# Performance work log

Hardware: AMD Instinct MI355X
Metric: run time of the kernel (lower is better)

The kernel has to match this reference:

```python
import jax, jax.numpy as jnp
import numpy as np

NUM_HEADS = 16


def setup_inputs() -> dict:
    key = jax.random.key(0)
    kx, kp, kq, kw, kb = jax.random.split(key, 5)
    B, N, C = 2, 2048, 1024
    x = jax.random.normal(kx, (B, N, C), dtype=jnp.float32)
    padding_mask = jax.random.randint(kp, (B, N), 0, 2).astype(jnp.bool_)
    W_qkv = jax.random.normal(kq, (C, 3 * C), dtype=jnp.float32) * (C ** -0.5)
    W_proj = jax.random.normal(kw, (C, C), dtype=jnp.float32) * (C ** -0.5)
    b_proj = jax.random.normal(kb, (C,), dtype=jnp.float32) * 0.02
    return {"x": x, "padding_mask": padding_mask, "causal_start": 128,
            "W_qkv": W_qkv, "W_proj": W_proj, "b_proj": b_proj}


def reference(x, padding_mask, causal_start, W_qkv, W_proj, b_proj):
    B, N, C = x.shape
    H = NUM_HEADS
    d = C // H
    scale = d ** -0.5
    # qkv projection: (B,N,3C) -> (3,B,H,N,d)
    qkv = (x @ W_qkv).reshape(B, N, 3, H, d).transpose(2, 0, 3, 1, 4)
    q, k, v = qkv[0], qkv[1], qkv[2]
    attn = jnp.einsum("bhqd,bhkd->bhqk", q * scale, k)  # (B,H,N,N)
    # padding mask: mask out padded KEY positions
    attn = jnp.where(padding_mask[:, None, None, :], -jnp.inf, attn)
    # offset causal mask: lower-triangular, but first `causal_start` columns always visible
    allowed = jnp.tril(jnp.ones((N, N), dtype=jnp.bool_))
    allowed = allowed | (jnp.arange(N)[None, :] < causal_start)
    attn = jnp.where(~allowed[None, None, :, :], -jnp.inf, attn)
    attn = jax.nn.softmax(attn.astype(jnp.float32), axis=-1).astype(x.dtype)
    out = jnp.einsum("bhqk,bhkd->bhqd", attn, v)  # (B,H,N,d)
    out = out.transpose(0, 2, 1, 3).reshape(B, N, C)
    return out @ W_proj + b_proj
```

## Files before the change

kernel.cpp:

```cpp
#include <hip/hip_runtime.h>
#include <stdint.h>

typedef unsigned short ushort_t;
typedef __attribute__((ext_vector_type(4))) unsigned short ushort4_t;
typedef __attribute__((ext_vector_type(8))) short short8;
typedef __attribute__((ext_vector_type(4))) float float4_t;

#define AS1 __attribute__((address_space(1)))
#define AS3 __attribute__((address_space(3)))

__device__ inline ushort_t f2bf(float f) {
    unsigned x = __builtin_bit_cast(unsigned, f);
    unsigned r = x + 0x7fffu + ((x >> 16) & 1u);
    return (ushort_t)(r >> 16);
}
__device__ inline ushort_t f2bf_trunc(float f) {
    return (ushort_t)(__builtin_bit_cast(unsigned, f) >> 16);
}

__global__ __launch_bounds__(256) void prep_fused(
    const float* __restrict__ wqkv, const float* __restrict__ x,
    const int* __restrict__ pad, const float* __restrict__ wproj,
    ushort_t* __restrict__ wqkvT, ushort_t* __restrict__ xbf,
    int* __restrict__ tbl, ushort_t* __restrict__ wprojT) {
    __shared__ __align__(16) ushort_t tile[64][65];
    __shared__ int wsum[4];
    int bid = blockIdx.x, t = threadIdx.x;
    if (bid < 768) {
        int bx = bid % 48, by = bid / 48;
        int c0 = bx * 64, r0 = by * 64;
        for (int i = 0; i < 16; i++) {
            int idx = t + i * 256;
            int lr = idx >> 6, lc = idx & 63;
            tile[lr][lc] = f2bf(wqkv[(size_t)(r0 + lr) * 3072 + c0 + lc]);
        }
        __syncthreads();
        for (int i = 0; i < 16; i++) {
            int idx = t + i * 256;
            int lr = idx >> 6, lc = idx & 63;
            wqkvT[(size_t)(c0 + lr) * 1024 + r0 + lc] = tile[lc][lr];
        }
    } else if (bid < 2816) {
        size_t i = ((size_t)(bid - 768) * 256 + t) * 8;
        float4_t a = *(const float4_t*)(x + i);
        float4_t b = *(const float4_t*)(x + i + 4);
        ushort_t u[8];
        u[0] = f2bf(a.x); u[1] = f2bf(a.y); u[2] = f2bf(a.z); u[3] = f2bf(a.w);
        u[4] = f2bf(b.x); u[5] = f2bf(b.y); u[6] = f2bf(b.z); u[7] = f2bf(b.w);
        *(ushort4_t*)(xbf + i) = *(ushort4_t*)&u[0];
        *(ushort4_t*)(xbf + i + 4) = *(ushort4_t*)&u[4];
    } else if (bid < 2818) {
        int b = bid - 2816;
        int* cvtab = tbl;
        int* pref = tbl + 4096;
        int* idxmap = tbl + 8192;
        int* vcp = tbl + 12288;
        int lane = t & 63, w4 = t >> 6;
        int base0 = t * 8;
        int v[8], s8 = 0;
        for (int j = 0; j < 8; j++) {
            v[j] = (pad[b * 2048 + base0 + j] == 0) ? 1 : 0;
            s8 += v[j];
        }
        int incl = s8;
        for (int off = 1; off < 64; off <<= 1) {
            int y = __shfl_up(incl, off, 64);
            if (lane >= off) incl += y;
        }
        int excl = incl - s8;
        if (lane == 63) wsum[w4] = incl;
        __syncthreads();
        int wbase = 0;
        for (int ww = 0; ww < 4; ww++) if (ww < w4) wbase += wsum[ww];
        int vcall = wsum[0] + wsum[1] + wsum[2] + wsum[3];
        int run = wbase + excl;
        for (int j = 0; j < 8; j++) {
            int pos = base0 + j;
            pref[b * 2048 + pos] = run;
            cvtab[b * 2048 + pos] = v[j] ? run : -1;
            if (v[j]) idxmap[b * 2048 + run] = pos;
            run += v[j];
        }
        if (t == 0) vcp[b] = vcall;
        for (int s = vcall + t; s < 2048; s += 256) idxmap[b * 2048 + s] = 2048;
    } else {
        int tid2 = bid - 2818;
        int c0 = (tid2 & 15) * 64, r0 = (tid2 >> 4) * 64;
        for (int i = 0; i < 16; i++) {
            int idx = t + i * 256;
            int lr = idx >> 6, lc = idx & 63;
            tile[lr][lc] = f2bf(wproj[(size_t)(r0 + lr) * 1024 + c0 + lc]);
        }
        __syncthreads();
        for (int i = 0; i < 16; i++) {
            int idx = t + i * 256;
            int lr = idx >> 6, lc = idx & 63;
            wprojT[(size_t)(c0 + lr) * 1024 + r0 + lc] = tile[lc][lr];
        }
    }
}

__global__ __launch_bounds__(256) void transpose_f32_bf16(const float* __restrict__ in,
                                                          ushort_t* __restrict__ out,
                                                          int R, int C) {
    __shared__ __align__(16) ushort_t tile[64][65];
    int c0 = blockIdx.x * 64, r0 = blockIdx.y * 64;
    int t = threadIdx.x;
    for (int i = 0; i < 16; i++) {
        int idx = t + i * 256;
        int lr = idx >> 6, lc = idx & 63;
        tile[lr][lc] = f2bf(in[(size_t)(r0 + lr) * C + c0 + lc]);
    }
    __syncthreads();
    for (int i = 0; i < 16; i++) {
        int idx = t + i * 256;
        int lr = idx >> 6, lc = idx & 63;
        out[(size_t)(c0 + lr) * R + r0 + lc] = tile[lc][lr];
    }
}

__global__ __launch_bounds__(256) void gemm_qkv(
    const ushort_t* __restrict__ A, const ushort_t* __restrict__ Bt,
    const int* __restrict__ tbl,
    ushort_t* __restrict__ outQ, ushort_t* __restrict__ outK, ushort_t* __restrict__ outV) {
    const int K = 1024;
    __shared__ __align__(16) ushort_t As[128 * 64];
    __shared__ __align__(16) ushort_t Bs[128 * 64];
    const int* idxmap = tbl + 8192;
    const int* vcp = tbl + 12288;
    int t = threadIdx.x;
    int w = t >> 6, lane = t & 63;
    int quad = lane >> 4, l15 = lane & 15;
    int wM = w >> 1, wN = w & 1;
    int lrow = lane >> 3;
    int lcol8 = (lane & 7) * 8;

    int wid = blockIdx.x + 24 * blockIdx.y;
    bool isQ = wid < 256;
    int b = 0, m0, vc = 0, tNr;
    size_t arow[4];
    if (isQ) {
        tNr = (wid & 7) * 128;
        m0 = (wid >> 3) * 128;
        for (int i = 0; i < 4; i++)
            arow[i] = (size_t)(m0 + w * 32 + i * 8 + lrow) * K;
    } else {
        int idx = wid - 256;
        int grp = idx >> 8;
        int r = idx & 255;
        int xkv = r >> 4;
        b = (r >> 3) & 1;
        int st = (r & 7) + grp * 8;
        tNr = 1024 + xkv * 128;
        vc = vcp[b];
        m0 = st * 128;
        if (m0 >= vc) return;
        for (int i = 0; i < 4; i++) {
            int slot = m0 + w * 32 + i * 8 + lrow;
            int orig = idxmap[b * 2048 + slot];
            arow[i] = (size_t)(b * 2048 + orig) * K;
        }
    }

    float4_t acc[4][4];
    for (int i = 0; i < 4; i++)
        for (int j = 0; j < 4; j++) acc[i][j] = (float4_t){0.f, 0.f, 0.f, 0.f};

    const ushort_t* Bbase = Bt + (size_t)(tNr + w * 32) * K;

    for (int k0 = 0; k0 < K; k0 += 64) {
        __syncthreads();
        for (int i = 0; i < 4; i++) {
            const ushort_t* ga = A + arow[i] + k0 + lcol8;
            __builtin_amdgcn_global_load_lds((AS1 void*)ga, (AS3 void*)&As[(w * 32 + i * 8) * 64], 16, 0, 0);
            const ushort_t* gb = Bbase + (size_t)(i * 8 + lrow) * K + k0 + lcol8;
            __builtin_amdgcn_global_load_lds((AS1 void*)gb, (AS3 void*)&Bs[(w * 32 + i * 8) * 64], 16, 0, 0);
        }
        __syncthreads();
        for (int kt = 0; kt < 2; kt++) {
            short8 af[4], bf[4];
            for (int m = 0; m < 4; m++)
                af[m] = *(const short8*)&As[(wM * 64 + m * 16 + l15) * 64 + kt * 32 + quad * 8];
            for (int n = 0; n < 4; n++)
                bf[n] = *(const short8*)&Bs[(wN * 64 + n * 16 + l15) * 64 + kt * 32 + quad * 8];
            for (int m = 0; m < 4; m++)
                for (int n = 0; n < 4; n++)
                    acc[m][n] = __builtin_amdgcn_mfma_f32_16x16x32_bf16(af[m], bf[n], acc[m][n], 0, 0, 0);
        }
    }

    for (int m = 0; m < 4; m++) {
        int lm = wM * 64 + m * 16 + quad * 4;
        for (int n = 0; n < 4; n++) {
            int lnc = wN * 64 + n * 16 + l15;
            if (isQ) {
                int gn = tNr + lnc;
                int h = gn >> 6, dd = gn & 63;
                for (int r = 0; r < 4; r++) {
                    int row = m0 + lm + r;
                    int bb = row >> 11, ns = row & 2047;
                    outQ[(((size_t)(bb * 16 + h) * 2048 + ns) << 6) + dd] = f2bf(acc[m][n][r]);
                }
            } else {
                int gnc = tNr - 1024 + lnc;
                ushort_t* dst = (gnc < 1024) ? outK : outV;
                int hh = (gnc >> 6) & 15, dd = gnc & 63;
                for (int r = 0; r < 4; r++) {
                    int slot = m0 + lm + r;
                    if (slot < vc)
                        dst[(((size_t)(b * 16 + hh) * 2048 + slot) << 6) + dd] = f2bf(acc[m][n][r]);
                }
            }
        }
    }
}

__global__ __launch_bounds__(512, 4) void attn_kernel(
    const ushort_t* __restrict__ q, const ushort_t* __restrict__ k,
    const ushort_t* __restrict__ v, const int* __restrict__ tbl,
    const int* __restrict__ csp, ushort_t* __restrict__ out) {
    __shared__ __align__(16) ushort_t Ks[2][64 * 64];
    __shared__ __align__(16) ushort_t VsT[2][64 * 64];
    __shared__ __align__(16) ushort_t Ps[8][16 * 64];
    __shared__ int Idx[2048];

    const int* pref = tbl + 4096;
    const int* idxmap = tbl + 8192;
    const int* vcp = tbl + 12288;

    int cs = csp[0];
    int t = threadIdx.x, w = t >> 6, lane = t & 63;
    int quad = lane >> 4, l15 = lane & 15;
    int bh = blockIdx.y;
    int b = bh >> 4, h = bh & 15;
    int g = (blockIdx.y < 16) ? blockIdx.x : 15 - blockIdx.x;
    int q0 = g * 128;
    int rowmin = q0 + w * 16;
    const float c1 = 0.18033688f;
    const float c2 = -11.541560f;

    int bound = q0 + 128; if (cs > bound) bound = cs;
    int nvalid = (bound > 2047) ? vcp[b] : pref[b * 2048 + bound];
    int nT = (nvalid + 63) >> 6; if (nT < 1) nT = 1;

    for (int i = 0; i < 4; i++) Idx[t + i * 512] = idxmap[b * 2048 + t + i * 512];

    const ushort_t* qb = q + ((size_t)bh * 2048 + rowmin + l15) * 64;
    short8 qf0 = *(const short8*)(qb + quad * 8);
    short8 qf1 = *(const short8*)(qb + 32 + quad * 8);

    float4_t O[4];
    for (int i = 0; i < 4; i++) O[i] = (float4_t){0.f, 0.f, 0.f, 0.f};
    float ls[4] = {0.f, 0.f, 0.f, 0.f};

    const ushort_t* kbase = k + (size_t)bh * 2048 * 64;
    const ushort_t* vbase = v + (size_t)bh * 2048 * 64;

    int lrow = lane >> 3, lblk = lane & 7;
    int prow = rowmin + quad * 4;
    int sw = l15 & 7;

    short8 vr;
    auto stageK = [&](int it, int buf) {
        int k0 = it * 64;
        const ushort_t* gk = kbase + (size_t)(k0 + w * 8 + lrow) * 64 + ((lblk ^ lrow) * 8);
        __builtin_amdgcn_global_load_lds((AS1 void*)gk, (AS3 void*)&Ks[buf][w * 8 * 64], 16, 0, 0);
    };
    auto loadV = [&](int it) {
        vr = *(const short8*)(vbase + (size_t)(it * 64 + lane) * 64 + w * 8);
        if (it * 64 + lane >= nvalid)
            for (int j = 0; j < 8; j++) vr[j] = 0;
    };

    stageK(0, 0);
    loadV(0);

    for (int it = 0; it < nT; it++) {
        int cur = it & 1, nxt = cur ^ 1;
        for (int j = 0; j < 8; j++) {
            int sl = ((lrow ^ j) * 8) + lblk;
            VsT[cur][(w * 8 + j) * 64 + sl] = (ushort_t)vr[j];
        }
        __syncthreads();
        if (it + 1 < nT) {
            stageK(it + 1, nxt);
            loadV(it + 1);
        }

        int k0 = it * 64;
        int omin = Idx[k0];
        bool act = (omin <= rowmin + 15) || (omin < cs);
        if (act) {
            int omax = Idx[k0 + 63];
            bool needC = (omax > rowmin) && (omax >= cs);

            short8 kf0[4], kf1[4];
            for (int ks = 0; ks < 4; ks++) {
                const ushort_t* krow = &Ks[cur][(ks * 16 + l15) * 64];
                kf0[ks] = *(const short8*)(krow + (quad ^ sw) * 8);
                kf1[ks] = *(const short8*)(krow + ((4 + quad) ^ sw) * 8);
            }

            float4_t s[4];
            for (int ks = 0; ks < 4; ks++) {
                float4_t a = (float4_t){0.f, 0.f, 0.f, 0.f};
                a = __builtin_amdgcn_mfma_f32_16x16x32_bf16(qf0, kf0[ks], a, 0, 0, 0);
                a = __builtin_amdgcn_mfma_f32_16x16x32_bf16(qf1, kf1[ks], a, 0, 0, 0);
                s[ks] = a;
            }
            for (int ks = 0; ks < 4; ks++) {
                int key = Idx[k0 + ks * 16 + l15];
                for (int r = 0; r < 4; r++) {
                    float arg = s[ks][r] * c1 + c2;
                    if (needC && (key > prow + r) && (key >= cs)) arg = -1e38f;
                    float p = __builtin_amdgcn_exp2f(arg);
                    ls[r] += p;
                    int row = quad * 4 + r;
                    Ps[w][row * 64 + (((ks * 2 + (l15 >> 3)) ^ (row & 7)) * 8) + (l15 & 7)] = f2bf_trunc(p);
                }
            }

            short8 vf0[4], vf1[4];
            for (int n = 0; n < 4; n++) {
                const ushort_t* vrow = &VsT[cur][(n * 16 + l15) * 64];
                vf0[n] = *(const short8*)(vrow + (quad ^ sw) * 8);
                vf1[n] = *(const short8*)(vrow + ((4 + quad) ^ sw) * 8);
            }
            const ushort_t* prl = &Ps[w][l15 * 64];
            short8 pf0 = *(const short8*)(prl + (quad ^ sw) * 8);
            short8 pf1 = *(const short8*)(prl + ((4 + quad) ^ sw) * 8);
            for (int n = 0; n < 4; n++) {
                O[n] = __builtin_amdgcn_mfma_f32_16x16x32_bf16(pf0, vf0[n], O[n], 0, 0, 0);
                O[n] = __builtin_amdgcn_mfma_f32_16x16x32_bf16(pf1, vf1[n], O[n], 0, 0, 0);
            }
        }
    }

    for (int r = 0; r < 4; r++) {
        float l = ls[r];
        l += __shfl_xor(l, 1, 64); l += __shfl_xor(l, 2, 64);
        l += __shfl_xor(l, 4, 64); l += __shfl_xor(l, 8, 64);
        float inv = l > 0.f ? 1.f / l : 0.f;
        int row = rowmin + quad * 4 + r;
        size_t ob = ((size_t)b * 2048 + row) * 1024 + h * 64;
        for (int n = 0; n < 4; n++)
            out[ob + n * 16 + l15] = f2bf(O[n][r] * inv);
    }
}

__global__ __launch_bounds__(256) void gemm_out_k(
    const ushort_t* __restrict__ A, const ushort_t* __restrict__ Bt,
    const float* __restrict__ bias, float* __restrict__ outC) {
    const int K = 1024, N = 1024;
    __shared__ __align__(16) ushort_t As[128 * 64];
    __shared__ __align__(16) ushort_t Bs[128 * 64];
    int t = threadIdx.x;
    int w = t >> 6, lane = t & 63;
    int quad = lane >> 4, l15 = lane & 15;
    int wM = w >> 1, wN = w & 1;
    int tM = blockIdx.y * 128, tN = blockIdx.x * 128;

    float4_t acc[4][4];
    for (int i = 0; i < 4; i++)
        for (int j = 0; j < 4; j++) acc[i][j] = (float4_t){0.f, 0.f, 0.f, 0.f};

    int lrow = lane >> 3;
    int lcol8 = (lane & 7) * 8;

    const ushort_t* Abase = A + (size_t)(tM + w * 32) * K;
    const ushort_t* Bbase = Bt + (size_t)(tN + w * 32) * K;

    for (int k0 = 0; k0 < K; k0 += 64) {
        __syncthreads();
        for (int i = 0; i < 4; i++) {
            const ushort_t* ga = Abase + (size_t)(i * 8 + lrow) * K + k0 + lcol8;
            __builtin_amdgcn_global_load_lds((AS1 void*)ga, (AS3 void*)&As[(w * 32 + i * 8) * 64], 16, 0, 0);
            const ushort_t* gb = Bbase + (size_t)(i * 8 + lrow) * K + k0 + lcol8;
            __builtin_amdgcn_global_load_lds((AS1 void*)gb, (AS3 void*)&Bs[(w * 32 + i * 8) * 64], 16, 0, 0);
        }
        __syncthreads();
        for (int kt = 0; kt < 2; kt++) {
            short8 af[4], bf[4];
            for (int m = 0; m < 4; m++)
                af[m] = *(const short8*)&As[(wM * 64 + m * 16 + l15) * 64 + kt * 32 + quad * 8];
            for (int n = 0; n < 4; n++)
                bf[n] = *(const short8*)&Bs[(wN * 64 + n * 16 + l15) * 64 + kt * 32 + quad * 8];
            for (int m = 0; m < 4; m++)
                for (int n = 0; n < 4; n++)
                    acc[m][n] = __builtin_amdgcn_mfma_f32_16x16x32_bf16(af[m], bf[n], acc[m][n], 0, 0, 0);
        }
    }

    for (int m = 0; m < 4; m++) {
        int gm = tM + wM * 64 + m * 16 + quad * 4;
        for (int n = 0; n < 4; n++) {
            int gn = tN + wN * 64 + n * 16 + l15;
            float bv = bias[gn];
            for (int r = 0; r < 4; r++)
                outC[(size_t)(gm + r) * N + gn] = acc[m][n][r] + bv;
        }
    }
}

extern "C" void kernel_launch(void* const* d_in, const int* in_sizes, int n_in,
                              void* d_out, int out_size, void* d_ws, size_t ws_size,
                              hipStream_t stream) {
    const float* x = (const float*)d_in[0];
    const int* pad = (const int*)d_in[1];
    const int* cs = (const int*)d_in[2];
    const float* wqkv = (const float*)d_in[3];
    const float* wproj = (const float*)d_in[4];
    const float* bproj = (const float*)d_in[5];
    float* out = (float*)d_out;

    ushort_t* ws = (ushort_t*)d_ws;
    ushort_t* qws = ws;
    ushort_t* kws = ws + (size_t)4194304;
    ushort_t* vws = ws + (size_t)8388608;
    ushort_t* wqkvT = ws + (size_t)12582912;
    ushort_t* aows = ws + (size_t)12582912;
    ushort_t* xbf = (ushort_t*)d_out;
    int* tbl = (int*)((char*)d_out + 8388608);

    bool fused_wp = ws_size >= (size_t)34 * 1024 * 1024;
    ushort_t* wprojT = fused_wp ? ws + (size_t)16777216 : ws;

    prep_fused<<<fused_wp ? 3074 : 2818, 256, 0, stream>>>(wqkv, x, pad, wproj,
                                                           wqkvT, xbf, tbl, wprojT);
    gemm_qkv<<<dim3(24, 32), 256, 0, stream>>>(xbf, wqkvT, tbl, qws, kws, vws);
    attn_kernel<<<dim3(16, 32), 512, 0, stream>>>(qws, kws, vws, tbl, cs, aows);
    if (!fused_wp)
        transpose_f32_bf16<<<dim3(16, 16), 256, 0, stream>>>(wproj, wprojT, 1024, 1024);
    gemm_out_k<<<dim3(8, 32), 256, 0, stream>>>(aows, wprojT, bproj, out);
}
```

Baseline: 175.3 us.

## Split K across two wave groups in projection GEMMs with LDS reduction

Both the QKV and output-projection GEMMs now launch 512-thread blocks. Two groups of four waves each handle one half of the K dimension in separate LDS buffers, then combine their partial accumulators through shared memory before the epilogue. This doubles the waves per tile to improve latency hiding and halves the serial K loop per wave. The cost is twice the LDS per block (64KB), an extra reduction step with two barriers, and possibly lower block-level occupancy.

After: 174.5 us. Within noise of the previous version (-0.5%).

```diff
diff --git a/kernel.cpp b/kernel.cpp
--- a/kernel.cpp
+++ b/kernel.cpp
@@ -119,19 +119,19 @@
     }
 }
 
-__global__ __launch_bounds__(256) void gemm_qkv(
+__global__ __launch_bounds__(512, 4) void gemm_qkv(
     const ushort_t* __restrict__ A, const ushort_t* __restrict__ Bt,
     const int* __restrict__ tbl,
     ushort_t* __restrict__ outQ, ushort_t* __restrict__ outK, ushort_t* __restrict__ outV) {
     const int K = 1024;
-    __shared__ __align__(16) ushort_t As[128 * 64];
-    __shared__ __align__(16) ushort_t Bs[128 * 64];
+    __shared__ __align__(16) ushort_t smem[4][128 * 64];
     const int* idxmap = tbl + 8192;
     const int* vcp = tbl + 12288;
     int t = threadIdx.x;
     int w = t >> 6, lane = t & 63;
+    int wq = w & 3, kh = w >> 2;
     int quad = lane >> 4, l15 = lane & 15;
-    int wM = w >> 1, wN = w & 1;
+    int wM = wq >> 1, wN = wq & 1;
     int lrow = lane >> 3;
     int lcol8 = (lane & 7) * 8;
 
@@ -143,7 +143,7 @@
         tNr = (wid & 7) * 128;
         m0 = (wid >> 3) * 128;
         for (int i = 0; i < 4; i++)
-            arow[i] = (size_t)(m0 + w * 32 + i * 8 + lrow) * K;
+            arow[i] = (size_t)(m0 + wq * 32 + i * 8 + lrow) * K;
     } else {
         int idx = wid - 256;
         int grp = idx >> 8;
@@ -156,7 +156,7 @@
         m0 = st * 128;
         if (m0 >= vc) return;
         for (int i = 0; i < 4; i++) {
-            int slot = m0 + w * 32 + i * 8 + lrow;
+            int slot = m0 + wq * 32 + i * 8 + lrow;
             int orig = idxmap[b * 2048 + slot];
             arow[i] = (size_t)(b * 2048 + orig) * K;
         }
@@ -166,28 +166,45 @@
     for (int i = 0; i < 4; i++)
         for (int j = 0; j < 4; j++) acc[i][j] = (float4_t){0.f, 0.f, 0.f, 0.f};
 
-    const ushort_t* Bbase = Bt + (size_t)(tNr + w * 32) * K;
-
-    for (int k0 = 0; k0 < K; k0 += 64) {
+    const ushort_t* Bbase = Bt + (size_t)(tNr + wq * 32) * K;
+    const int kb = kh * 512;
+
+    for (int k0 = 0; k0 < 512; k0 += 64) {
         __syncthreads();
         for (int i = 0; i < 4; i++) {
-            const ushort_t* ga = A + arow[i] + k0 + lcol8;
-            __builtin_amdgcn_global_load_lds((AS1 void*)ga, (AS3 void*)&As[(w * 32 + i * 8) * 64], 16, 0, 0);
-            const ushort_t* gb = Bbase + (size_t)(i * 8 + lrow) * K + k0 + lcol8;
-            __builtin_amdgcn_global_load_lds((AS1 void*)gb, (AS3 void*)&Bs[(w * 32 + i * 8) * 64], 16, 0, 0);
+            const ushort_t* ga = A + arow[i] + kb + k0 + lcol8;
+            __builtin_amdgcn_global_load_lds((AS1 void*)ga, (AS3 void*)&smem[kh][(wq * 32 + i * 8) * 64], 16, 0, 0);
+            const ushort_t* gb = Bbase + (size_t)(i * 8 + lrow) * K + kb + k0 + lcol8;
+            __builtin_amdgcn_global_load_lds((AS1 void*)gb, (AS3 void*)&smem[2 + kh][(wq * 32 + i * 8) * 64], 16, 0, 0);
         }
         __syncthreads();
         for (int kt = 0; kt < 2; kt++) {
             short8 af[4], bf[4];
             for (int m = 0; m < 4; m++)
-                af[m] = *(const short8*)&As[(wM * 64 + m * 16 + l15) * 64 + kt * 32 + quad * 8];
+                af[m] = *(const short8*)&smem[kh][(wM * 64 + m * 16 + l15) * 64 + kt * 32 + quad * 8];
             for (int n = 0; n < 4; n++)
-                bf[n] = *(const short8*)&Bs[(wN * 64 + n * 16 + l15) * 64 + kt * 32 + quad * 8];
+                bf[n] = *(const short8*)&smem[2 + kh][(wN * 64 + n * 16 + l15) * 64 + kt * 32 + quad * 8];
             for (int m = 0; m < 4; m++)
                 for (int n = 0; n < 4; n++)
                     acc[m][n] = __builtin_amdgcn_mfma_f32_16x16x32_bf16(af[m], bf[n], acc[m][n], 0, 0, 0);
         }
     }
+
+    __syncthreads();
+    float4_t* red = (float4_t*)smem;
+    if (kh == 1) {
+        for (int m = 0; m < 4; m++)
+            for (int n = 0; n < 4; n++)
+                red[(wq * 16 + m * 4 + n) * 64 + lane] = acc[m][n];
+    }
+    __syncthreads();
+    if (kh == 1) return;
+    for (int m = 0; m < 4; m++)
+        for (int n = 0; n < 4; n++) {
+            float4_t o = red[(wq * 16 + m * 4 + n) * 64 + lane];
+            acc[m][n].x += o.x; acc[m][n].y += o.y;
+            acc[m][n].z += o.z; acc[m][n].w += o.w;
+        }
 
     for (int m = 0; m < 4; m++) {
         int lm = wM * 64 + m * 16 + quad * 4;
@@ -348,16 +365,16 @@
     }
 }
 
-__global__ __launch_bounds__(256) void gemm_out_k(
+__global__ __launch_bounds__(512, 4) void gemm_out_k(
     const ushort_t* __restrict__ A, const ushort_t* __restrict__ Bt,
     const float* __restrict__ bias, float* __restrict__ outC) {
     const int K = 1024, N = 1024;
-    __shared__ __align__(16) ushort_t As[128 * 64];
-    __shared__ __align__(16) ushort_t Bs[128 * 64];
+    __shared__ __align__(16) ushort_t smem[4][128 * 64];
     int t = threadIdx.x;
     int w = t >> 6, lane = t & 63;
+    int wq = w & 3, kh = w >> 2;
     int quad = lane >> 4, l15 = lane & 15;
-    int wM = w >> 1, wN = w & 1;
+    int wM = wq >> 1, wN = wq & 1;
     int tM = blockIdx.y * 128, tN = blockIdx.x * 128;
 
     float4_t acc[4][4];
@@ -367,29 +384,46 @@
     int lrow = lane >> 3;
     int lcol8 = (lane & 7) * 8;
 
-    const ushort_t* Abase = A + (size_t)(tM + w * 32) * K;
-    const ushort_t* Bbase = Bt + (size_t)(tN + w * 32) * K;
-
-    for (int k0 = 0; k0 < K; k0 += 64) {
+    const ushort_t* Abase = A + (size_t)(tM + wq * 32) * K;
+    const ushort_t* Bbase = Bt + (size_t)(tN + wq * 32) * K;
+    const int kb = kh * 512;
+
+    for (int k0 = 0; k0 < 512; k0 += 64) {
         __syncthreads();
         for (int i = 0; i < 4; i++) {
-            const ushort_t* ga = Abase + (size_t)(i * 8 + lrow) * K + k0 + lcol8;
-            __builtin_amdgcn_global_load_lds((AS1 void*)ga, (AS3 void*)&As[(w * 32 + i * 8) * 64], 16, 0, 0);
-            const ushort_t* gb = Bbase + (size_t)(i * 8 + lrow) * K + k0 + lcol8;
-            __builtin_amdgcn_global_load_lds((AS1 void*)gb, (AS3 void*)&Bs[(w * 32 + i * 8) * 64], 16, 0, 0);
+            const ushort_t* ga = Abase + (size_t)(i * 8 + lrow) * K + kb + k0 + lcol8;
+            __builtin_amdgcn_global_load_lds((AS1 void*)ga, (AS3 void*)&smem[kh][(wq * 32 + i * 8) * 64], 16, 0, 0);
+            const ushort_t* gb = Bbase + (size_t)(i * 8 + lrow) * K + kb + k0 + lcol8;
+            __builtin_amdgcn_global_load_lds((AS1 void*)gb, (AS3 void*)&smem[2 + kh][(wq * 32 + i * 8) * 64], 16, 0, 0);
         }
         __syncthreads();
         for (int kt = 0; kt < 2; kt++) {
             short8 af[4], bf[4];
             for (int m = 0; m < 4; m++)
-                af[m] = *(const short8*)&As[(wM * 64 + m * 16 + l15) * 64 + kt * 32 + quad * 8];
+                af[m] = *(const short8*)&smem[kh][(wM * 64 + m * 16 + l15) * 64 + kt * 32 + quad * 8];
             for (int n = 0; n < 4; n++)
-                bf[n] = *(const short8*)&Bs[(wN * 64 + n * 16 + l15) * 64 + kt * 32 + quad * 8];
+                bf[n] = *(const short8*)&smem[2 + kh][(wN * 64 + n * 16 + l15) * 64 + kt * 32 + quad * 8];
             for (int m = 0; m < 4; m++)
                 for (int n = 0; n < 4; n++)
                     acc[m][n] = __builtin_amdgcn_mfma_f32_16x16x32_bf16(af[m], bf[n], acc[m][n], 0, 0, 0);
         }
     }
+
+    __syncthreads();
+    float4_t* red = (float4_t*)smem;
+    if (kh == 1) {
+        for (int m = 0; m < 4; m++)
+            for (int n = 0; n < 4; n++)
+                red[(wq * 16 + m * 4 + n) * 64 + lane] = acc[m][n];
+    }
+    __syncthreads();
+    if (kh == 1) return;
+    for (int m = 0; m < 4; m++)
+        for (int n = 0; n < 4; n++) {
+            float4_t o = red[(wq * 16 + m * 4 + n) * 64 + lane];
+            acc[m][n].x += o.x; acc[m][n].y += o.y;
+            acc[m][n].z += o.z; acc[m][n].w += o.w;
+        }
 
     for (int m = 0; m < 4; m++) {
         int gm = tM + wM * 64 + m * 16 + quad * 4;
@@ -427,9 +461,9 @@
 
     prep_fused<<<fused_wp ? 3074 : 2818, 256, 0, stream>>>(wqkv, x, pad, wproj,
                                                            wqkvT, xbf, tbl, wprojT);
-    gemm_qkv<<<dim3(24, 32), 256, 0, stream>>>(xbf, wqkvT, tbl, qws, kws, vws);
+    gemm_qkv<<<dim3(24, 32), 512, 0, stream>>>(xbf, wqkvT, tbl, qws, kws, vws);
     attn_kernel<<<dim3(16, 32), 512, 0, stream>>>(qws, kws, vws, tbl, cs, aows);
     if (!fused_wp)
         transpose_f32_bf16<<<dim3(16, 16), 256, 0, stream>>>(wproj, wprojT, 1024, 1024);
-    gemm_out_k<<<dim3(8, 32), 256, 0, stream>>>(aows, wprojT, bproj, out);
-}
+    gemm_out_k<<<dim3(8, 32), 512, 0, stream>>>(aows, wprojT, bproj, out);
+}
```

## Double-buffer LDS tiles in QKV and output projection GEMMs

Applied to the files above, without the earlier changes.

Both GEMM kernels now hold two LDS buffers for the A and B tiles. The next K-slice is prefetched with global_load_lds into the alternate buffer while MFMAs run on the current one, which cuts the per-iteration barriers from two to one. The aim is to hide global-to-LDS latency behind matrix compute. In exchange, LDS use per block doubles to 64KB, which may lower the number of blocks resident per CU.

Result: slower. 183.3 us (+4.6%).

```diff
diff --git a/kernel.cpp b/kernel.cpp
--- a/kernel.cpp
+++ b/kernel.cpp
@@ -124,8 +124,8 @@
     const int* __restrict__ tbl,
     ushort_t* __restrict__ outQ, ushort_t* __restrict__ outK, ushort_t* __restrict__ outV) {
     const int K = 1024;
-    __shared__ __align__(16) ushort_t As[128 * 64];
-    __shared__ __align__(16) ushort_t Bs[128 * 64];
+    __shared__ __align__(16) ushort_t As[2][128 * 64];
+    __shared__ __align__(16) ushort_t Bs[2][128 * 64];
     const int* idxmap = tbl + 8192;
     const int* vcp = tbl + 12288;
     int t = threadIdx.x;
@@ -168,21 +168,27 @@
 
     const ushort_t* Bbase = Bt + (size_t)(tNr + w * 32) * K;
 
-    for (int k0 = 0; k0 < K; k0 += 64) {
-        __syncthreads();
+    auto stage = [&](int ks, int buf) {
+        int k0 = ks * 64;
         for (int i = 0; i < 4; i++) {
             const ushort_t* ga = A + arow[i] + k0 + lcol8;
-            __builtin_amdgcn_global_load_lds((AS1 void*)ga, (AS3 void*)&As[(w * 32 + i * 8) * 64], 16, 0, 0);
+            __builtin_amdgcn_global_load_lds((AS1 void*)ga, (AS3 void*)&As[buf][(w * 32 + i * 8) * 64], 16, 0, 0);
             const ushort_t* gb = Bbase + (size_t)(i * 8 + lrow) * K + k0 + lcol8;
-            __builtin_amdgcn_global_load_lds((AS1 void*)gb, (AS3 void*)&Bs[(w * 32 + i * 8) * 64], 16, 0, 0);
-        }
-        __syncthreads();
+            __builtin_amdgcn_global_load_lds((AS1 void*)gb, (AS3 void*)&Bs[buf][(w * 32 + i * 8) * 64], 16, 0, 0);
+        }
+    };
+
+    stage(0, 0);
+    for (int ks = 0; ks < 16; ks++) {
+        int cur = ks & 1;
+        __syncthreads();
+        if (ks + 1 < 16) stage(ks + 1, cur ^ 1);
         for (int kt = 0; kt < 2; kt++) {
             short8 af[4], bf[4];
             for (int m = 0; m < 4; m++)
-                af[m] = *(const short8*)&As[(wM * 64 + m * 16 + l15) * 64 + kt * 32 + quad * 8];
+                af[m] = *(const short8*)&As[cur][(wM * 64 + m * 16 + l15) * 64 + kt * 32 + quad * 8];
             for (int n = 0; n < 4; n++)
-                bf[n] = *(const short8*)&Bs[(wN * 64 + n * 16 + l15) * 64 + kt * 32 + quad * 8];
+                bf[n] = *(const short8*)&Bs[cur][(wN * 64 + n * 16 + l15) * 64 + kt * 32 + quad * 8];
             for (int m = 0; m < 4; m++)
                 for (int n = 0; n < 4; n++)
                     acc[m][n] = __builtin_amdgcn_mfma_f32_16x16x32_bf16(af[m], bf[n], acc[m][n], 0, 0, 0);
@@ -352,8 +358,8 @@
     const ushort_t* __restrict__ A, const ushort_t* __restrict__ Bt,
     const float* __restrict__ bias, float* __restrict__ outC) {
     const int K = 1024, N = 1024;
-    __shared__ __align__(16) ushort_t As[128 * 64];
-    __shared__ __align__(16) ushort_t Bs[128 * 64];
+    __shared__ __align__(16) ushort_t As[2][128 * 64];
+    __shared__ __align__(16) ushort_t Bs[2][128 * 64];
     int t = threadIdx.x;
     int w = t >> 6, lane = t & 63;
     int quad = lane >> 4, l15 = lane & 15;
@@ -370,21 +376,27 @@
     const ushort_t* Abase = A + (size_t)(tM + w * 32) * K;
     const ushort_t* Bbase = Bt + (size_t)(tN + w * 32) * K;
 
-    for (int k0 = 0; k0 < K; k0 += 64) {
-        __syncthreads();
+    auto stage = [&](int ks, int buf) {
+        int k0 = ks * 64;
         for (int i = 0; i < 4; i++) {
             const ushort_t* ga = Abase + (size_t)(i * 8 + lrow) * K + k0 + lcol8;
-            __builtin_amdgcn_global_load_lds((AS1 void*)ga, (AS3 void*)&As[(w * 32 + i * 8) * 64], 16, 0, 0);
+            __builtin_amdgcn_global_load_lds((AS1 void*)ga, (AS3 void*)&As[buf][(w * 32 + i * 8) * 64], 16, 0, 0);
             const ushort_t* gb = Bbase + (size_t)(i * 8 + lrow) * K + k0 + lcol8;
-            __builtin_amdgcn_global_load_lds((AS1 void*)gb, (AS3 void*)&Bs[(w * 32 + i * 8) * 64], 16, 0, 0);
-        }
-        __syncthreads();
+            __builtin_amdgcn_global_load_lds((AS1 void*)gb, (AS3 void*)&Bs[buf][(w * 32 + i * 8) * 64], 16, 0, 0);
+        }
+    };
+
+    stage(0, 0);
+    for (int ks = 0; ks < 16; ks++) {
+        int cur = ks & 1;
+        __syncthreads();
+        if (ks + 1 < 16) stage(ks + 1, cur ^ 1);
         for (int kt = 0; kt < 2; kt++) {
             short8 af[4], bf[4];
             for (int m = 0; m < 4; m++)
-                af[m] = *(const short8*)&As[(wM * 64 + m * 16 + l15) * 64 + kt * 32 + quad * 8];
+                af[m] = *(const short8*)&As[cur][(wM * 64 + m * 16 + l15) * 64 + kt * 32 + quad * 8];
             for (int n = 0; n < 4; n++)
-                bf[n] = *(const short8*)&Bs[(wN * 64 + n * 16 + l15) * 64 + kt * 32 + quad * 8];
+                bf[n] = *(const short8*)&Bs[cur][(wN * 64 + n * 16 + l15) * 64 + kt * 32 + quad * 8];
             for (int m = 0; m < 4; m++)
                 for (int n = 0; n < 4; n++)
                     acc[m][n] = __builtin_amdgcn_mfma_f32_16x16x32_bf16(af[m], bf[n], acc[m][n], 0, 0, 0);
```
